# Kernel optimization log

Hardware: AMD Instinct MI355X
Metric: run time of the kernel (lower is better)

## Reference

```python
import jax, jax.numpy as jnp
import numpy as np

INV_LN2 = 1.4426950408889634  # 1 / ln(2)
MAGIC = jnp.int16(24375)      # Quake-style magic constant for bf16


def _isqrt_bf16(x):
    """Fast inverse sqrt: bf16 bit-trick initial guess + one Newton step, all in bf16."""
    y = x.astype(jnp.bfloat16)
    i = jax.lax.bitcast_convert_type(y, jnp.int16)
    i = (MAGIC - (i >> 1)).astype(jnp.int16)          # arithmetic shift, int16 wrap
    y = jax.lax.bitcast_convert_type(i, jnp.bfloat16)  # initial estimate
    y2 = (y * y).astype(jnp.bfloat16)
    xh = (x * jnp.bfloat16(0.5)).astype(jnp.bfloat16)
    mul = (xh * y2).astype(jnp.bfloat16)
    sub = (jnp.bfloat16(1.5) - mul).astype(jnp.bfloat16)
    return (y * sub).astype(jnp.bfloat16)              # one Newton-Raphson iteration


def setup_inputs() -> dict:
    key = jax.random.key(0)
    x = jax.random.normal(key, (2, 16, 2048, 2048), dtype=jnp.float32)
    return {"x": x}


def reference(x) -> jnp.ndarray:
    # q = floor(x / ln2), exp approx = 2**q  (power-of-two quantized exp)
    q = jnp.floor(x * INV_LN2).astype(jnp.bfloat16)
    exp_x = jnp.exp2(q).astype(jnp.bfloat16)
    exp_sum = jnp.sum(exp_x, axis=-1, keepdims=True).astype(jnp.bfloat16)
    r = _isqrt_bf16(exp_sum)                           # 1/sqrt(sum)
    out = exp_x * r * r                                # exp_x / sum  via (1/sqrt)^2
    return out.astype(jnp.float32)
```

## Files before the change

### kernel.cpp

```cpp
#include <hip/hip_runtime.h>
#include <hip/hip_bf16.h>
#include <stdint.h>


#define INV_LN2F 1.4426950408889634f

__device__ __forceinline__ float rne_bf16(float f) {
    uint32_t u = __float_as_uint(f);
    uint32_t r = (u + 0x7FFFu + ((u >> 16) & 1u)) & 0xFFFF0000u;
    return __uint_as_float(r);
}

__global__ __launch_bounds__(256) void hmq_softmax_kernel(
        const float* __restrict__ x, float* __restrict__ out) {
    const int row = blockIdx.x;
    const int t = threadIdx.x;
    const size_t base = (size_t)row * 2048;

    const float4* __restrict__ xr = (const float4*)(x + base);
    float4 a = xr[t];
    float4 b = xr[256 + t];

    float v[8] = {a.x, a.y, a.z, a.w, b.x, b.y, b.z, b.w};
    float e[8];
    float partial = 0.0f;
    #pragma unroll
    for (int k = 0; k < 8; ++k) {
        float m = floorf(v[k] * INV_LN2F);
        float ev = ldexpf(1.0f, (int)m);
        e[k] = ev;
        partial += ev;
    }

    #pragma unroll
    for (int off = 32; off > 0; off >>= 1)
        partial += __shfl_xor(partial, off, 64);

    __shared__ float ws[4];
    __shared__ float rsh;
    const int wave = t >> 6;
    if ((t & 63) == 0) ws[wave] = partial;
    __syncthreads();
    if (t == 0) {
        float s  = (ws[0] + ws[1]) + (ws[2] + ws[3]);
        float sb = rne_bf16(s);

        uint16_t bits = (uint16_t)(__float_as_uint(sb) >> 16);
        int16_t  i    = (int16_t)bits;
        i = (int16_t)(24375 - (i >> 1));
        float y   = __uint_as_float(((uint32_t)(uint16_t)i) << 16);
        float y2  = rne_bf16(y * y);
        float xh  = rne_bf16(sb * 0.5f);
        float mul = rne_bf16(xh * y2);
        float sub = rne_bf16(1.5f - mul);
        rsh = rne_bf16(y * sub);
    }
    __syncthreads();
    const float r = rsh;

    float o[8];
    #pragma unroll
    for (int k = 0; k < 8; ++k) {
        float tt = rne_bf16(e[k] * r);
        o[k]     = rne_bf16(tt * r);
    }

    float4* __restrict__ orow = (float4*)(out + base);
    orow[t]       = make_float4(o[0], o[1], o[2], o[3]);
    orow[256 + t] = make_float4(o[4], o[5], o[6], o[7]);
}

extern "C" void kernel_launch(void* const* d_in, const int* in_sizes, int n_in,
                              void* d_out, int out_size, void* d_ws, size_t ws_size,
                              hipStream_t stream) {
    (void)n_in; (void)d_ws; (void)ws_size; (void)out_size;
    const float* x = (const float*)d_in[0];
    float* out = (float*)d_out;
    const int rows = in_sizes[0] / 2048;
    hmq_softmax_kernel<<<rows, 256, 0, stream>>>(x, out);
}
```

Before: 187.0 us.

## Assign one row per wavefront and use nontemporal vector loads/stores

Each 64-lane wave now handles a whole 2048-element row, so the row sum is a pure shuffle reduction with no shared memory or block barriers. Each block covers four rows, which cuts the grid size by four. Loads and stores use nontemporal builtins to stream data past the cache. Each thread now holds 32 values, which raises register pressure and reduces the loads in flight per element.

```diff
diff --git a/kernel.cpp b/kernel.cpp
--- a/kernel.cpp
+++ b/kernel.cpp
@@ -4,6 +4,8 @@
 
 
 #define INV_LN2F 1.4426950408889634f
+
+typedef float f32x4 __attribute__((ext_vector_type(4)));
 
 __device__ __forceinline__ float rne_bf16(float f) {
     uint32_t u = __float_as_uint(f);
@@ -13,61 +15,57 @@
 
 __global__ __launch_bounds__(256) void hmq_softmax_kernel(
         const float* __restrict__ x, float* __restrict__ out) {
-    const int row = blockIdx.x;
-    const int t = threadIdx.x;
-    const size_t base = (size_t)row * 2048;
+    const int wave = threadIdx.x >> 6;
+    const int lane = threadIdx.x & 63;
+    const size_t row = (size_t)blockIdx.x * 4 + wave;
+    const size_t base = row * 2048;
 
-    const float4* __restrict__ xr = (const float4*)(x + base);
-    float4 a = xr[t];
-    float4 b = xr[256 + t];
+    const f32x4* __restrict__ xr = (const f32x4*)(x + base);
+    f32x4* __restrict__ orow = (f32x4*)(out + base);
 
-    float v[8] = {a.x, a.y, a.z, a.w, b.x, b.y, b.z, b.w};
-    float e[8];
+    f32x4 v[8];
+    #pragma unroll
+    for (int c = 0; c < 8; ++c)
+        v[c] = __builtin_nontemporal_load(&xr[c * 64 + lane]);
+
+    float e[32];
     float partial = 0.0f;
     #pragma unroll
-    for (int k = 0; k < 8; ++k) {
-        float m = floorf(v[k] * INV_LN2F);
-        float ev = ldexpf(1.0f, (int)m);
-        e[k] = ev;
-        partial += ev;
+    for (int c = 0; c < 8; ++c) {
+        #pragma unroll
+        for (int k = 0; k < 4; ++k) {
+            float m  = floorf(v[c][k] * INV_LN2F);
+            float ev = ldexpf(1.0f, (int)m);
+            e[c * 4 + k] = ev;
+            partial += ev;
+        }
     }
 
     #pragma unroll
     for (int off = 32; off > 0; off >>= 1)
         partial += __shfl_xor(partial, off, 64);
 
-    __shared__ float ws[4];
-    __shared__ float rsh;
-    const int wave = t >> 6;
-    if ((t & 63) == 0) ws[wave] = partial;
-    __syncthreads();
-    if (t == 0) {
-        float s  = (ws[0] + ws[1]) + (ws[2] + ws[3]);
-        float sb = rne_bf16(s);
+    float sb = rne_bf16(partial);
+    uint16_t bits = (uint16_t)(__float_as_uint(sb) >> 16);
+    int16_t  i    = (int16_t)bits;
+    i = (int16_t)(24375 - (i >> 1));
+    float y   = __uint_as_float(((uint32_t)(uint16_t)i) << 16);
+    float y2  = rne_bf16(y * y);
+    float xh  = rne_bf16(sb * 0.5f);
+    float mul = rne_bf16(xh * y2);
+    float sub = rne_bf16(1.5f - mul);
+    float r   = rne_bf16(y * sub);
 
-        uint16_t bits = (uint16_t)(__float_as_uint(sb) >> 16);
-        int16_t  i    = (int16_t)bits;
-        i = (int16_t)(24375 - (i >> 1));
-        float y   = __uint_as_float(((uint32_t)(uint16_t)i) << 16);
-        float y2  = rne_bf16(y * y);
-        float xh  = rne_bf16(sb * 0.5f);
-        float mul = rne_bf16(xh * y2);
-        float sub = rne_bf16(1.5f - mul);
-        rsh = rne_bf16(y * sub);
+    #pragma unroll
+    for (int c = 0; c < 8; ++c) {
+        f32x4 o;
+        #pragma unroll
+        for (int k = 0; k < 4; ++k) {
+            float tt = rne_bf16(e[c * 4 + k] * r);
+            o[k]     = rne_bf16(tt * r);
+        }
+        __builtin_nontemporal_store(o, &orow[c * 64 + lane]);
     }
-    __syncthreads();
-    const float r = rsh;
-
-    float o[8];
-    #pragma unroll
-    for (int k = 0; k < 8; ++k) {
-        float tt = rne_bf16(e[k] * r);
-        o[k]     = rne_bf16(tt * r);
-    }
-
-    float4* __restrict__ orow = (float4*)(out + base);
-    orow[t]       = make_float4(o[0], o[1], o[2], o[3]);
-    orow[256 + t] = make_float4(o[4], o[5], o[6], o[7]);
 }
 
 extern "C" void kernel_launch(void* const* d_in, const int* in_sizes, int n_in,
@@ -77,5 +75,5 @@
     const float* x = (const float*)d_in[0];
     float* out = (float*)d_out;
     const int rows = in_sizes[0] / 2048;
-    hmq_softmax_kernel<<<rows, 256, 0, stream>>>(x, out);
+    hmq_softmax_kernel<<<rows / 4, 256, 0, stream>>>(x, out);
 }
```

New measurement: 176.6 us. 5.5% less time.
